# Kernel optimization log

Hardware: AMD Instinct MI355X
Metric: run time of the kernel (lower is better)

## Reference

```python
import jax, jax.numpy as jnp
import numpy as np
from jax import lax

K = 3          # kernel_size
STRIDE = 1
PAD = 1        # (K-1)//2
C = 64         # channels
GC = 16        # group_channels
G = C // GC    # groups = 4
NS = 1         # new_size = ratio * stride
EPS = 1e-5


def mish(x):
    return x * jnp.tanh(jax.nn.softplus(x))


def setup_inputs() -> dict:
    key = jax.random.key(0)
    ks = jax.random.split(key, 4)
    B, H, W = 2, 256, 256
    c1_in = C * K * 2 + G * K * K      # 420
    c1_out = C * NS * NS // 4          # 16
    return {
        "inputs": jax.random.normal(ks[0], (B, C, H, W), jnp.float32),
        "conv1_w": jax.random.normal(ks[1], (c1_out, c1_in, 1, 1), jnp.float32) * 0.05,
        "conv1_b": jnp.zeros((c1_out,), jnp.float32),
        "conv2_w": jax.random.normal(ks[2], (C // 4, C // 4, 3, 3), jnp.float32) * 0.05,
        "conv2_b": jnp.zeros((C // 4,), jnp.float32),
        "conv3_w": jax.random.normal(ks[3], (G * K * K, C // 4, 1, 1), jnp.float32) * 0.05,
        "conv3_b": jnp.zeros((G * K * K,), jnp.float32),
        "bn_gamma": jnp.ones((c1_out,), jnp.float32),
        "bn_beta": jnp.zeros((c1_out,), jnp.float32),
        "bn_mean": jnp.zeros((c1_out,), jnp.float32),
        "bn_var": jnp.ones((c1_out,), jnp.float32),
    }


def _unfold(x, h, w):
    # torch.nn.Unfold(K, 1, PAD, STRIDE): output channel layout (C, kh, kw)
    xp = jnp.pad(x, ((0, 0), (0, 0), (PAD, PAD), (PAD, PAD)))
    cols = [xp[:, :, ki:ki + (h - 1) * STRIDE + 1:STRIDE,
                     kj:kj + (w - 1) * STRIDE + 1:STRIDE]
            for ki in range(K) for kj in range(K)]
    return jnp.stack(cols, axis=2)  # (b, C, K*K, h, w)


def reference(inputs, conv1_w, conv1_b, conv2_w, conv2_b, conv3_w, conv3_b,
              bn_gamma, bn_beta, bn_mean, bn_var):
    b, _, Wd, Hd = inputs.shape
    h = (Wd + 2 * PAD - K) // STRIDE + 1
    w = (Hd + 2 * PAD - K) // STRIDE + 1
    x = _unfold(inputs, h, w).reshape(b, G, GC, K, K, h, w)
    # multi-axis max pooling over (group_channels, kh, kw)
    m_gc = x.max(axis=2).reshape(b, -1, h, w)  # (b, G*K*K, h, w)
    m_kh = x.max(axis=3).reshape(b, -1, h, w)  # (b, C*K, h, w)
    m_kw = x.max(axis=4).reshape(b, -1, h, w)  # (b, C*K, h, w)
    weight = jnp.concatenate([m_gc, m_kh, m_kw], axis=1)  # (b, 420, h, w)
    # conv1 (1x1) + Mish
    weight = mish(jnp.einsum('bihw,oi->bohw', weight, conv1_w[:, :, 0, 0])
                  + conv1_b[None, :, None, None])                  # (b, 16, h, w)
    c = C // 4
    # rearrange 'b (c n1 n2) h w -> (b h w) c n1 n2'
    wn = weight.reshape(b, c, NS, NS, h, w).transpose(0, 4, 5, 1, 2, 3)
    wn = wn.reshape(b * h * w, c, NS, NS)
    wn = lax.conv_general_dilated(wn, conv2_w, (1, 1), ((1, 1), (1, 1)),
                                  dimension_numbers=('NCHW', 'OIHW', 'NCHW'))
    wn = wn + conv2_b[None, :, None, None]
    # rearrange back '(b h w) c n1 n2 -> b (c n1 n2) h w'
    wn = wn.reshape(b, h, w, c, NS, NS).transpose(0, 3, 4, 5, 1, 2)
    wn = wn.reshape(b, c * NS * NS, h, w)
    # BatchNorm (inference form with running stats)
    scale = bn_gamma / jnp.sqrt(bn_var + EPS)
    wn = wn * scale[None, :, None, None] + (bn_beta - bn_mean * scale)[None, :, None, None]
    weight = weight * mish(wn)
    # conv3 (1x1) -> per-pixel attention logits
    weight = jnp.einsum('bihw,oi->bohw', weight, conv3_w[:, :, 0, 0]) \
             + conv3_b[None, :, None, None]                          # (b, G*K*K, h, w)
    weight = jax.nn.softmax(weight.reshape(b, G, 1, K * K, NS * NS, h, w), axis=3)
    # softmax-weighted patch aggregation
    agg = jnp.sum(x.reshape(b, G, GC, K * K, 1, h, w) * weight, axis=3)  # (b,G,GC,NS^2,h,w)
    # fold with kernel=stride=NS (non-overlapping): pure reshape/transpose
    out = agg.reshape(b, C, NS, NS, h, w).transpose(0, 1, 4, 2, 5, 3)
    return out.reshape(b, C, h * NS, w * NS)
```

## Files before the change

kernel.cpp:

```cpp
#include <hip/hip_runtime.h>
#include <math.h>

#define Cch 64
#define Hh  256
#define Ww  256

#define WS_WPA   0
#define WS_WGC   6144
#define WS_WC2   6720
#define WS_SC    6976
#define WS_OFF   6992
#define WS_FLOATS 7008

__device__ __forceinline__ float mishf(float x) {
    float e  = __expf(fminf(x, 15.0f));
    float n  = 1.0f + e;
    float n2 = n * n;
    float t  = __fdividef(n2 - 1.0f, n2 + 1.0f);
    return x > 15.0f ? x : x * t;
}

__global__ __launch_bounds__(256) void prep_kernel(
    const float* __restrict__ w1, const float* __restrict__ w2,
    const float* __restrict__ b2,
    const float* __restrict__ gamma, const float* __restrict__ beta,
    const float* __restrict__ mean,  const float* __restrict__ var,
    float* __restrict__ ws)
{
    for (int idx = threadIdx.x; idx < 6144; idx += 256) {
        int c = idx / 96, r = idx % 96, o = r / 6, j = r % 6;
        float v = (j < 3) ? w1[o * 420 + 36 + c * 3 + j]
                          : w1[o * 420 + 228 + c * 3 + (j - 3)];
        ws[WS_WPA + idx] = v;
    }
    for (int idx = threadIdx.x; idx < 576; idx += 256) {
        int g = idx / 144, rem = idx % 144, o = rem / 9, k = rem % 9;
        ws[WS_WGC + idx] = w1[o * 420 + g * 9 + k];
    }
    for (int idx = threadIdx.x; idx < 256; idx += 256) {
        int o = idx / 16, i = idx % 16;
        ws[WS_WC2 + idx] = w2[o * 144 + i * 9 + 4];
    }
    if (threadIdx.x < 16) {
        int o = threadIdx.x;
        float sc = gamma[o] * rsqrtf(var[o] + 1e-5f);
        ws[WS_SC + o]  = sc;
        ws[WS_OFF + o] = b2[o] * sc + beta[o] - mean[o] * sc;
    }
}

__global__ __launch_bounds__(256, 4) void revo_kernel(
    const float* __restrict__ in,
    const float* __restrict__ b1,
    const float* __restrict__ w3, const float* __restrict__ b3,
    const float* __restrict__ ws,
    float* __restrict__ out)
{
    const int tid  = threadIdx.x;
    const int g    = __builtin_amdgcn_readfirstlane(tid >> 6);
    const int lane = tid & 63;

    const int bid     = blockIdx.x;
    const int logical = ((bid & 7) << 8) + (bid >> 3);
    const int wseg = logical & 3;
    const int h    = (logical >> 2) & (Hh - 1);
    const int b    = logical >> 10;

    const int w = wseg * 64 + lane;

    __shared__ float lds_y[4][64][17];

    const float* base = in + (size_t)b * Cch * Hh * Ww;

    const bool okm = (w > 0);
    const bool okp = (w < Ww - 1);
    const int offm = okm ? -1 : 0;
    const int offp = okp ?  1 : 0;

    const int hm = h - 1, hp = h + 1;
    const bool okhm = (hm >= 0), okhp = (hp < Hh);
    const int hmc = okhm ? hm : 0;
    const int hpc = okhp ? hp : Hh - 1;

    float y[16];
    #pragma unroll
    for (int o = 0; o < 16; ++o) y[o] = 0.0f;
    float gmax[9];

    const float* wpA = ws + WS_WPA + (size_t)(g << 4) * 96;

    float p[9], pn[9];
    {
        const float* cb = base + (size_t)(g << 4) * Hh * Ww;
        const float* r0 = cb + (size_t)hmc * Ww + w;
        const float* r1 = cb + (size_t)h   * Ww + w;
        const float* r2 = cb + (size_t)hpc * Ww + w;
        p[0] = r0[offm]; p[1] = r0[0]; p[2] = r0[offp];
        p[3] = r1[offm]; p[4] = r1[0]; p[5] = r1[offp];
        p[6] = r2[offm]; p[7] = r2[0]; p[8] = r2[offp];
    }

    for (int cc = 0; cc < 16; ++cc) {
        if (cc < 15) {
            const float* cb = base + (size_t)((g << 4) + cc + 1) * Hh * Ww;
            const float* r0 = cb + (size_t)hmc * Ww + w;
            const float* r1 = cb + (size_t)h   * Ww + w;
            const float* r2 = cb + (size_t)hpc * Ww + w;
            pn[0] = r0[offm]; pn[1] = r0[0]; pn[2] = r0[offp];
            pn[3] = r1[offm]; pn[4] = r1[0]; pn[5] = r1[offp];
            pn[6] = r2[offm]; pn[7] = r2[0]; pn[8] = r2[offp];
        }

        float q[9];
        q[0] = (okhm && okm) ? p[0] : 0.0f;
        q[1] =  okhm         ? p[1] : 0.0f;
        q[2] = (okhm && okp) ? p[2] : 0.0f;
        q[3] =  okm          ? p[3] : 0.0f;
        q[4] =  p[4];
        q[5] =  okp          ? p[5] : 0.0f;
        q[6] = (okhp && okm) ? p[6] : 0.0f;
        q[7] =  okhp         ? p[7] : 0.0f;
        q[8] = (okhp && okp) ? p[8] : 0.0f;

        float mkh0 = fmaxf(fmaxf(q[0], q[3]), q[6]);
        float mkh1 = fmaxf(fmaxf(q[1], q[4]), q[7]);
        float mkh2 = fmaxf(fmaxf(q[2], q[5]), q[8]);
        float mkw0 = fmaxf(fmaxf(q[0], q[1]), q[2]);
        float mkw1 = fmaxf(fmaxf(q[3], q[4]), q[5]);
        float mkw2 = fmaxf(fmaxf(q[6], q[7]), q[8]);

        if (cc == 0) {
            #pragma unroll
            for (int k = 0; k < 9; ++k) gmax[k] = q[k];
        } else {
            #pragma unroll
            for (int k = 0; k < 9; ++k) gmax[k] = fmaxf(gmax[k], q[k]);
        }

        const float* r = wpA + cc * 96;
        #pragma unroll
        for (int o = 0; o < 16; ++o) {
            y[o] = fmaf(r[o * 6 + 0], mkh0, y[o]);
            y[o] = fmaf(r[o * 6 + 1], mkh1, y[o]);
            y[o] = fmaf(r[o * 6 + 2], mkh2, y[o]);
            y[o] = fmaf(r[o * 6 + 3], mkw0, y[o]);
            y[o] = fmaf(r[o * 6 + 4], mkw1, y[o]);
            y[o] = fmaf(r[o * 6 + 5], mkw2, y[o]);
        }

        #pragma unroll
        for (int k = 0; k < 9; ++k) p[k] = pn[k];
    }
    {
        const float* r = ws + WS_WGC + g * 144;
        #pragma unroll
        for (int o = 0; o < 16; ++o)
            #pragma unroll
            for (int k = 0; k < 9; ++k)
                y[o] = fmaf(r[o * 9 + k], gmax[k], y[o]);
    }

    #pragma unroll
    for (int o = 0; o < 16; ++o) lds_y[g][lane][o] = y[o];
    __syncthreads();

    float feat[16];
    #pragma unroll
    for (int o = 0; o < 16; ++o) {
        float t = lds_y[0][lane][o] + lds_y[1][lane][o]
                + lds_y[2][lane][o] + lds_y[3][lane][o] + b1[o];
        feat[o] = mishf(t);
    }

    float feat2[16];
    {
        const float* wc2 = ws + WS_WC2;
        const float* sc  = ws + WS_SC;
        const float* off = ws + WS_OFF;
        #pragma unroll
        for (int o = 0; o < 16; ++o) {
            float acc = 0.0f;
            #pragma unroll
            for (int i = 0; i < 16; ++i)
                acc = fmaf(wc2[o * 16 + i], feat[i], acc);
            feat2[o] = feat[o] * mishf(acc * sc[o] + off[o]);
        }
    }

    float att[9];
    {
        float mx = -1e30f;
        #pragma unroll
        for (int k = 0; k < 9; ++k) {
            float acc = b3[g * 9 + k];
            const float* r = w3 + (g * 9 + k) * 16;
            #pragma unroll
            for (int i = 0; i < 16; ++i)
                acc = fmaf(r[i], feat2[i], acc);
            att[k] = acc;
            mx = fmaxf(mx, acc);
        }
        float s = 0.0f;
        #pragma unroll
        for (int k = 0; k < 9; ++k) { att[k] = __expf(att[k] - mx); s += att[k]; }
        float inv = __fdividef(1.0f, s);
        #pragma unroll
        for (int k = 0; k < 9; ++k) att[k] *= inv;
    }

    float* ob = out + (((size_t)b * Cch) * Hh + h) * Ww + w;
    {
        const float* cb = base + (size_t)(g << 4) * Hh * Ww;
        const float* r0 = cb + (size_t)hmc * Ww + w;
        const float* r1 = cb + (size_t)h   * Ww + w;
        const float* r2 = cb + (size_t)hpc * Ww + w;
        p[0] = r0[offm]; p[1] = r0[0]; p[2] = r0[offp];
        p[3] = r1[offm]; p[4] = r1[0]; p[5] = r1[offp];
        p[6] = r2[offm]; p[7] = r2[0]; p[8] = r2[offp];
    }
    for (int gc = 0; gc < 16; ++gc) {
        if (gc < 15) {
            const float* cb = base + (size_t)((g << 4) + gc + 1) * Hh * Ww;
            const float* r0 = cb + (size_t)hmc * Ww + w;
            const float* r1 = cb + (size_t)h   * Ww + w;
            const float* r2 = cb + (size_t)hpc * Ww + w;
            pn[0] = r0[offm]; pn[1] = r0[0]; pn[2] = r0[offp];
            pn[3] = r1[offm]; pn[4] = r1[0]; pn[5] = r1[offp];
            pn[6] = r2[offm]; pn[7] = r2[0]; pn[8] = r2[offp];
        }
        float acc = 0.0f;
        acc = fmaf((okhm && okm) ? p[0] : 0.0f, att[0], acc);
        acc = fmaf( okhm         ? p[1] : 0.0f, att[1], acc);
        acc = fmaf((okhm && okp) ? p[2] : 0.0f, att[2], acc);
        acc = fmaf( okm          ? p[3] : 0.0f, att[3], acc);
        acc = fmaf( p[4],                       att[4], acc);
        acc = fmaf( okp          ? p[5] : 0.0f, att[5], acc);
        acc = fmaf((okhp && okm) ? p[6] : 0.0f, att[6], acc);
        acc = fmaf( okhp         ? p[7] : 0.0f, att[7], acc);
        acc = fmaf((okhp && okp) ? p[8] : 0.0f, att[8], acc);
        ob[(size_t)((g << 4) + gc) * Hh * Ww] = acc;

        #pragma unroll
        for (int k = 0; k < 9; ++k) p[k] = pn[k];
    }
}

extern "C" void kernel_launch(void* const* d_in, const int* in_sizes, int n_in,
                              void* d_out, int out_size, void* d_ws, size_t ws_size,
                              hipStream_t stream) {
    const float* in    = (const float*)d_in[0];
    const float* w1    = (const float*)d_in[1];
    const float* b1    = (const float*)d_in[2];
    const float* w2    = (const float*)d_in[3];
    const float* b2    = (const float*)d_in[4];
    const float* w3    = (const float*)d_in[5];
    const float* b3    = (const float*)d_in[6];
    const float* gamma = (const float*)d_in[7];
    const float* beta  = (const float*)d_in[8];
    const float* mean  = (const float*)d_in[9];
    const float* var   = (const float*)d_in[10];
    float* out = (float*)d_out;
    float* ws  = (float*)d_ws;

    hipLaunchKernelGGL(prep_kernel, dim3(1), dim3(256), 0, stream,
                       w1, w2, b2, gamma, beta, mean, var, ws);

    dim3 grid(2 * Hh * 4);
    dim3 block(256);
    hipLaunchKernelGGL(revo_kernel, grid, block, 0, stream,
                       in, b1, w3, b3, ws, out);
}
```

Baseline: 97.96 us.

## Move conv1 reduction onto bf16 MFMA with hi/lo split weights

The per-thread scalar FMA loop for conv1 (105 inputs × 16 outputs per group) is replaced by packing the max-pooled features as bf16 into swizzled LDS tiles and computing them with mfma_f32_16x16x32_bf16. Weights are split into hi and lo bf16 parts to recover precision, and the prep kernel lays them out per lane. The input prefetch is deepened to two channels ahead. The cost removed is VALU FMA work and scalar weight loads. In exchange the features are rounded to bf16, there is extra LDS traffic, and the launch-bounds occupancy hint is dropped.

```diff
diff --git a/kernel.cpp b/kernel.cpp
--- a/kernel.cpp
+++ b/kernel.cpp
@@ -1,16 +1,19 @@
 #include <hip/hip_runtime.h>
+#include <hip/hip_bf16.h>
 #include <math.h>
 
 #define Cch 64
 #define Hh  256
 #define Ww  256
-
-#define WS_WPA   0
-#define WS_WGC   6144
-#define WS_WC2   6720
-#define WS_SC    6976
-#define WS_OFF   6992
-#define WS_FLOATS 7008
+#define HW  (Hh * Ww)
+
+#define WS_WA   0
+#define WS_WC2  8192
+#define WS_SC   8448
+#define WS_OFF  8464
+
+typedef __attribute__((ext_vector_type(8))) short bf16x8;
+typedef __attribute__((ext_vector_type(4))) float f32x4;
 
 __device__ __forceinline__ float mishf(float x) {
     float e  = __expf(fminf(x, 15.0f));
@@ -18,6 +21,24 @@
     float n2 = n * n;
     float t  = __fdividef(n2 - 1.0f, n2 + 1.0f);
     return x > 15.0f ? x : x * t;
+}
+
+__device__ __forceinline__ unsigned packbf(float a, float b) {
+    unsigned short ua = __builtin_bit_cast(unsigned short, __float2bfloat16(a));
+    unsigned short ub = __builtin_bit_cast(unsigned short, __float2bfloat16(b));
+    return (unsigned)ua | ((unsigned)ub << 16);
+}
+
+__device__ __forceinline__ float conv1_wval(const float* w1, int g, int m, int k) {
+    if (k < 96) {
+        int cc = k / 6, r = k % 6;
+        int col = (r < 3) ? (36 + (g * 16 + cc) * 3 + r)
+                          : (228 + (g * 16 + cc) * 3 + (r - 3));
+        return w1[m * 420 + col];
+    } else if (k < 105) {
+        return w1[m * 420 + g * 9 + (k - 96)];
+    }
+    return 0.0f;
 }
 
 __global__ __launch_bounds__(256) void prep_kernel(
@@ -27,29 +48,53 @@
     const float* __restrict__ mean,  const float* __restrict__ var,
     float* __restrict__ ws)
 {
-    for (int idx = threadIdx.x; idx < 6144; idx += 256) {
-        int c = idx / 96, r = idx % 96, o = r / 6, j = r % 6;
-        float v = (j < 3) ? w1[o * 420 + 36 + c * 3 + j]
-                          : w1[o * 420 + 228 + c * 3 + (j - 3)];
-        ws[WS_WPA + idx] = v;
-    }
-    for (int idx = threadIdx.x; idx < 576; idx += 256) {
-        int g = idx / 144, rem = idx % 144, o = rem / 9, k = rem % 9;
-        ws[WS_WGC + idx] = w1[o * 420 + g * 9 + k];
-    }
-    for (int idx = threadIdx.x; idx < 256; idx += 256) {
+    unsigned* wsu = (unsigned*)ws;
+    const int tid = threadIdx.x;
+
+    for (int idx = tid; idx < 1024; idx += 256) {
+        int lane = idx & 63, s = (idx >> 6) & 3, g = idx >> 8;
+        int m = lane & 15, half = lane >> 4;
+        unsigned hi[4], lo[4];
+        #pragma unroll
+        for (int jp = 0; jp < 4; ++jp) {
+            float hv[2], lv[2];
+            #pragma unroll
+            for (int e = 0; e < 2; ++e) {
+                int k = 32 * s + half * 8 + jp * 2 + e;
+                float v  = conv1_wval(w1, g, m, k);
+                float hf = __bfloat162float(__float2bfloat16(v));
+                hv[e] = hf;
+                lv[e] = v - hf;
+            }
+            hi[jp] = packbf(hv[0], hv[1]);
+            lo[jp] = packbf(lv[0], lv[1]);
+        }
+        int b0 = WS_WA + idx * 8;
+        #pragma unroll
+        for (int i = 0; i < 4; ++i) { wsu[b0 + i] = hi[i]; wsu[b0 + 4 + i] = lo[i]; }
+    }
+
+    for (int idx = tid; idx < 256; idx += 256) {
         int o = idx / 16, i = idx % 16;
         ws[WS_WC2 + idx] = w2[o * 144 + i * 9 + 4];
     }
-    if (threadIdx.x < 16) {
-        int o = threadIdx.x;
-        float sc = gamma[o] * rsqrtf(var[o] + 1e-5f);
-        ws[WS_SC + o]  = sc;
-        ws[WS_OFF + o] = b2[o] * sc + beta[o] - mean[o] * sc;
-    }
-}
-
-__global__ __launch_bounds__(256, 4) void revo_kernel(
+    if (tid < 16) {
+        float sc = gamma[tid] * rsqrtf(var[tid] + 1e-5f);
+        ws[WS_SC + tid]  = sc;
+        ws[WS_OFF + tid] = b2[tid] * sc + beta[tid] - mean[tid] * sc;
+    }
+}
+
+#define LOAD9(dst, cb) do {                              \
+    const float* r0_ = (cb) + (size_t)hmc * Ww + w;      \
+    const float* r1_ = (cb) + (size_t)h   * Ww + w;      \
+    const float* r2_ = (cb) + (size_t)hpc * Ww + w;      \
+    dst[0] = r0_[offm]; dst[1] = r0_[0]; dst[2] = r0_[offp]; \
+    dst[3] = r1_[offm]; dst[4] = r1_[0]; dst[5] = r1_[offp]; \
+    dst[6] = r2_[offm]; dst[7] = r2_[0]; dst[8] = r2_[offp]; \
+} while (0)
+
+__global__ __launch_bounds__(256) void revo_kernel(
     const float* __restrict__ in,
     const float* __restrict__ b1,
     const float* __restrict__ w3, const float* __restrict__ b3,
@@ -58,19 +103,19 @@
 {
     const int tid  = threadIdx.x;
     const int g    = __builtin_amdgcn_readfirstlane(tid >> 6);
-    const int lane = tid & 63;
+    const int l    = tid & 63;
 
     const int bid     = blockIdx.x;
     const int logical = ((bid & 7) << 8) + (bid >> 3);
     const int wseg = logical & 3;
     const int h    = (logical >> 2) & (Hh - 1);
     const int b    = logical >> 10;
-
-    const int w = wseg * 64 + lane;
-
-    __shared__ float lds_y[4][64][17];
-
-    const float* base = in + (size_t)b * Cch * Hh * Ww;
+    const int w    = wseg * 64 + l;
+
+    __shared__ uint4 feats[4][64][16];
+    __shared__ f32x4 lds_y[4][64][4];
+
+    const float* base = in + (size_t)b * Cch * HW;
 
     const bool okm = (w > 0);
     const bool okp = (w < Ww - 1);
@@ -82,33 +127,17 @@
     const int hmc = okhm ? hm : 0;
     const int hpc = okhp ? hp : Hh - 1;
 
-    float y[16];
+    float p[9], pn[9], pnn[9];
+    float gmax[9];
+    unsigned pk[53];
+
+    LOAD9(p,  base + (size_t)(g * 16 + 0) * HW);
+    LOAD9(pn, base + (size_t)(g * 16 + 1) * HW);
+
     #pragma unroll
-    for (int o = 0; o < 16; ++o) y[o] = 0.0f;
-    float gmax[9];
-
-    const float* wpA = ws + WS_WPA + (size_t)(g << 4) * 96;
-
-    float p[9], pn[9];
-    {
-        const float* cb = base + (size_t)(g << 4) * Hh * Ww;
-        const float* r0 = cb + (size_t)hmc * Ww + w;
-        const float* r1 = cb + (size_t)h   * Ww + w;
-        const float* r2 = cb + (size_t)hpc * Ww + w;
-        p[0] = r0[offm]; p[1] = r0[0]; p[2] = r0[offp];
-        p[3] = r1[offm]; p[4] = r1[0]; p[5] = r1[offp];
-        p[6] = r2[offm]; p[7] = r2[0]; p[8] = r2[offp];
-    }
-
     for (int cc = 0; cc < 16; ++cc) {
-        if (cc < 15) {
-            const float* cb = base + (size_t)((g << 4) + cc + 1) * Hh * Ww;
-            const float* r0 = cb + (size_t)hmc * Ww + w;
-            const float* r1 = cb + (size_t)h   * Ww + w;
-            const float* r2 = cb + (size_t)hpc * Ww + w;
-            pn[0] = r0[offm]; pn[1] = r0[0]; pn[2] = r0[offp];
-            pn[3] = r1[offm]; pn[4] = r1[0]; pn[5] = r1[offp];
-            pn[6] = r2[offm]; pn[7] = r2[0]; pn[8] = r2[offp];
+        if (cc < 14) {
+            LOAD9(pnn, base + (size_t)(g * 16 + cc + 2) * HW);
         }
 
         float q[9];
@@ -137,39 +166,76 @@
             for (int k = 0; k < 9; ++k) gmax[k] = fmaxf(gmax[k], q[k]);
         }
 
-        const float* r = wpA + cc * 96;
-        #pragma unroll
-        for (int o = 0; o < 16; ++o) {
-            y[o] = fmaf(r[o * 6 + 0], mkh0, y[o]);
-            y[o] = fmaf(r[o * 6 + 1], mkh1, y[o]);
-            y[o] = fmaf(r[o * 6 + 2], mkh2, y[o]);
-            y[o] = fmaf(r[o * 6 + 3], mkw0, y[o]);
-            y[o] = fmaf(r[o * 6 + 4], mkw1, y[o]);
-            y[o] = fmaf(r[o * 6 + 5], mkw2, y[o]);
-        }
-
-        #pragma unroll
-        for (int k = 0; k < 9; ++k) p[k] = pn[k];
-    }
-    {
-        const float* r = ws + WS_WGC + g * 144;
+        pk[3 * cc + 0] = packbf(mkh0, mkh1);
+        pk[3 * cc + 1] = packbf(mkh2, mkw0);
+        pk[3 * cc + 2] = packbf(mkw1, mkw2);
+
+        #pragma unroll
+        for (int k = 0; k < 9; ++k) { p[k] = pn[k]; pn[k] = pnn[k]; }
+    }
+    pk[48] = packbf(gmax[0], gmax[1]);
+    pk[49] = packbf(gmax[2], gmax[3]);
+    pk[50] = packbf(gmax[4], gmax[5]);
+    pk[51] = packbf(gmax[6], gmax[7]);
+    pk[52] = packbf(gmax[8], 0.0f);
+
+    {
+        const int sw = l & 7;
+        #pragma unroll
+        for (int m = 0; m < 13; ++m) {
+            uint4 v; v.x = pk[4*m]; v.y = pk[4*m+1]; v.z = pk[4*m+2]; v.w = pk[4*m+3];
+            feats[g][l][m ^ sw] = v;
+        }
+        uint4 vt; vt.x = pk[52]; vt.y = 0u; vt.z = 0u; vt.w = 0u;
+        feats[g][l][13 ^ sw] = vt;
+        uint4 vz; vz.x = 0u; vz.y = 0u; vz.z = 0u; vz.w = 0u;
+        feats[g][l][14 ^ sw] = vz;
+        feats[g][l][15 ^ sw] = vz;
+    }
+
+    {
+        const uint4* wa = (const uint4*)ws;
+        uint4 Ahi[4], Alo[4];
+        #pragma unroll
+        for (int s = 0; s < 4; ++s) {
+            int ix = ((g * 4 + s) * 64 + l) * 2;
+            Ahi[s] = wa[ix];
+            Alo[s] = wa[ix + 1];
+        }
+
+        f32x4 acc[4];
+        #pragma unroll
+        for (int t = 0; t < 4; ++t) acc[t] = (f32x4){0.f, 0.f, 0.f, 0.f};
+
+        const int ln = l & 15, half = l >> 4, sw = l & 7;
+        #pragma unroll
+        for (int s = 0; s < 4; ++s) {
+            #pragma unroll
+            for (int t = 0; t < 4; ++t) {
+                uint4 bv = feats[g][16 * t + ln][(4 * s + half) ^ sw];
+                acc[t] = __builtin_amdgcn_mfma_f32_16x16x32_bf16(
+                    __builtin_bit_cast(bf16x8, Ahi[s]),
+                    __builtin_bit_cast(bf16x8, bv), acc[t], 0, 0, 0);
+                acc[t] = __builtin_amdgcn_mfma_f32_16x16x32_bf16(
+                    __builtin_bit_cast(bf16x8, Alo[s]),
+                    __builtin_bit_cast(bf16x8, bv), acc[t], 0, 0, 0);
+            }
+        }
+        #pragma unroll
+        for (int t = 0; t < 4; ++t)
+            lds_y[g][16 * t + ln][half] = acc[t];
+    }
+    __syncthreads();
+
+    float feat[16];
+    {
+        f32x4 rr[4];
+        #pragma unroll
+        for (int r = 0; r < 4; ++r)
+            rr[r] = lds_y[0][l][r] + lds_y[1][l][r] + lds_y[2][l][r] + lds_y[3][l][r];
         #pragma unroll
         for (int o = 0; o < 16; ++o)
-            #pragma unroll
-            for (int k = 0; k < 9; ++k)
-                y[o] = fmaf(r[o * 9 + k], gmax[k], y[o]);
-    }
-
-    #pragma unroll
-    for (int o = 0; o < 16; ++o) lds_y[g][lane][o] = y[o];
-    __syncthreads();
-
-    float feat[16];
-    #pragma unroll
-    for (int o = 0; o < 16; ++o) {
-        float t = lds_y[0][lane][o] + lds_y[1][lane][o]
-                + lds_y[2][lane][o] + lds_y[3][lane][o] + b1[o];
-        feat[o] = mishf(t);
+            feat[o] = mishf(rr[o >> 2][o & 3] + b1[o]);
     }
 
     float feat2[16];
@@ -209,24 +275,10 @@
     }
 
     float* ob = out + (((size_t)b * Cch) * Hh + h) * Ww + w;
-    {
-        const float* cb = base + (size_t)(g << 4) * Hh * Ww;
-        const float* r0 = cb + (size_t)hmc * Ww + w;
-        const float* r1 = cb + (size_t)h   * Ww + w;
-        const float* r2 = cb + (size_t)hpc * Ww + w;
-        p[0] = r0[offm]; p[1] = r0[0]; p[2] = r0[offp];
-        p[3] = r1[offm]; p[4] = r1[0]; p[5] = r1[offp];
-        p[6] = r2[offm]; p[7] = r2[0]; p[8] = r2[offp];
-    }
+    LOAD9(p, base + (size_t)(g * 16) * HW);
     for (int gc = 0; gc < 16; ++gc) {
         if (gc < 15) {
-            const float* cb = base + (size_t)((g << 4) + gc + 1) * Hh * Ww;
-            const float* r0 = cb + (size_t)hmc * Ww + w;
-            const float* r1 = cb + (size_t)h   * Ww + w;
-            const float* r2 = cb + (size_t)hpc * Ww + w;
-            pn[0] = r0[offm]; pn[1] = r0[0]; pn[2] = r0[offp];
-            pn[3] = r1[offm]; pn[4] = r1[0]; pn[5] = r1[offp];
-            pn[6] = r2[offm]; pn[7] = r2[0]; pn[8] = r2[offp];
+            LOAD9(pn, base + (size_t)(g * 16 + gc + 1) * HW);
         }
         float acc = 0.0f;
         acc = fmaf((okhm && okm) ? p[0] : 0.0f, att[0], acc);
@@ -238,7 +290,7 @@
         acc = fmaf((okhp && okm) ? p[6] : 0.0f, att[6], acc);
         acc = fmaf( okhp         ? p[7] : 0.0f, att[7], acc);
         acc = fmaf((okhp && okp) ? p[8] : 0.0f, att[8], acc);
-        ob[(size_t)((g << 4) + gc) * Hh * Ww] = acc;
+        ob[(size_t)(g * 16 + gc) * HW] = acc;
 
         #pragma unroll
         for (int k = 0; k < 9; ++k) p[k] = pn[k];
@@ -265,8 +317,6 @@
     hipLaunchKernelGGL(prep_kernel, dim3(1), dim3(256), 0, stream,
                        w1, w2, b2, gamma, beta, mean, var, ws);
 
-    dim3 grid(2 * Hh * 4);
-    dim3 block(256);
-    hipLaunchKernelGGL(revo_kernel, grid, block, 0, stream,
+    hipLaunchKernelGGL(revo_kernel, dim3(2048), dim3(256), 0, stream,
                        in, b1, w3, b3, ws, out);
 }
```

Result: no change. 96.16 us (-1.8%).
